# Kernel optimization log

Hardware: AMD Instinct MI355X
Metric: run time of the kernel (lower is better)

The kernel has to match this reference:

```python
import jax, jax.numpy as jnp
import numpy as np

D_MODEL = 1024
NUM_HEADS = 16
DEPTH = D_MODEL // NUM_HEADS


def setup_inputs() -> dict:
    key = jax.random.key(0)
    ks = jax.random.split(key, 10)
    B, LQ, LK = 4, 2048, 2048
    # xavier_uniform bound for square [d,d] weight
    bound = float(np.sqrt(6.0 / (D_MODEL + D_MODEL)))
    def w(k):
        return jax.random.uniform(k, (D_MODEL, D_MODEL), jnp.float32, -bound, bound)
    return {
        "query": jax.random.normal(ks[0], (B, LQ, D_MODEL), jnp.float32),
        "value": jax.random.normal(ks[1], (B, LK, D_MODEL), jnp.float32),
        "wq": w(ks[2]), "bq": jnp.zeros((D_MODEL,), jnp.float32),
        "wk": w(ks[3]), "bk": jnp.zeros((D_MODEL,), jnp.float32),
        "wv": w(ks[4]), "bv": jnp.zeros((D_MODEL,), jnp.float32),
        "wo": w(ks[5]), "bo": jnp.zeros((D_MODEL,), jnp.float32),
    }


def _split_heads(x, B):
    # [B, L, d_model] -> [B, H, L, depth]
    return x.reshape(B, -1, NUM_HEADS, DEPTH).transpose(0, 2, 1, 3)


def reference(query, value, wq, bq, wk, bk, wv, bv, wo, bo):
    B = query.shape[0]
    # torch nn.Linear: y = x @ W.T + b
    q = _split_heads(query @ wq.T + bq, B)          # [B,H,Lq,depth]
    k = _split_heads(value @ wk.T + bk, B)          # [B,H,Lk,depth]
    v = _split_heads(value @ wv.T + bv, B)          # [B,H,Lk,depth]
    scale = jnp.sqrt(jnp.asarray(DEPTH, dtype=q.dtype))
    scores = jnp.einsum("bhqd,bhkd->bhqk", q, k) / scale
    attn = jax.nn.softmax(scores, axis=-1)
    ctx = jnp.einsum("bhqk,bhkd->bhqd", attn, v)    # [B,H,Lq,depth]
    ctx = ctx.transpose(0, 2, 1, 3).reshape(B, -1, D_MODEL)
    return ctx @ wo.T + bo
```

## Files before the change

kernel.cpp:

```cpp
#include <hip/hip_runtime.h>
#include <hip/hip_bf16.h>

typedef unsigned short u16;
typedef unsigned int u32;
typedef __attribute__((ext_vector_type(8))) short bf16x8;
typedef __attribute__((ext_vector_type(4))) float f32x4;

#define MFMA16(a, b, c) __builtin_amdgcn_mfma_f32_16x16x32_bf16(a, b, c, 0, 0, 0)

#define QSCALE 0.18033688011112042f

__device__ inline u16 f2b(float f) {
    union { float f; unsigned int i; } v;
    v.f = f;
    unsigned int r = v.i + 0x7fffu + ((v.i >> 16) & 1u);
    return (u16)(r >> 16);
}
__device__ inline u32 fbits(float f) {
    union { float f; u32 i; } v; v.f = f; return v.i;
}
__device__ inline u32 pack2_trunc(float f0, float f1) {
    return __builtin_amdgcn_perm(fbits(f1), fbits(f0), 0x07060302u);
}

__device__ inline void glds16(const u16* g, u16* l) {
    __builtin_amdgcn_global_load_lds(
        (const __attribute__((address_space(1))) unsigned int*)g,
        (__attribute__((address_space(3))) unsigned int*)l, 16, 0, 0);
}

__global__ __launch_bounds__(256) void cvt_f32_bf16(
    const float* __restrict__ x, u16* __restrict__ y, int n)
{
    int i = (blockIdx.x * 256 + threadIdx.x) * 8;
    if (i >= n) return;
    float4 a = *(const float4*)(x + i);
    float4 b = *(const float4*)(x + i + 4);
    u16 o[8] = { f2b(a.x), f2b(a.y), f2b(a.z), f2b(a.w),
                 f2b(b.x), f2b(b.y), f2b(b.z), f2b(b.w) };
    *(uint4*)(y + i) = *(uint4*)o;
}

__global__ __launch_bounds__(256) void gemm_proj(
    const u16* __restrict__ qb, const u16* __restrict__ vb,
    const u16* __restrict__ wqb, const u16* __restrict__ wkb,
    const u16* __restrict__ wvb,
    const float* __restrict__ bq, const float* __restrict__ bk,
    const float* __restrict__ bv,
    u16* __restrict__ Qp, u16* __restrict__ Kp, u16* __restrict__ Vp,
    int M, int K)
{
    const int sel = blockIdx.y >> 3;
    const int n0 = (blockIdx.y & 7) * 128;
    const u16* A = sel ? vb : qb;
    const u16* W = sel == 0 ? wqb : (sel == 1 ? wkb : wvb);
    const float* bias = sel == 0 ? bq : (sel == 1 ? bk : bv);
    u16* C = sel == 0 ? Qp : (sel == 1 ? Kp : Vp);
    const float cscale = sel == 0 ? QSCALE : 1.0f;

    __shared__ __align__(16) u16 As[128 * 32];
    __shared__ __align__(16) u16 Bs[128 * 32];

    const int tid  = threadIdx.x;
    const int wave = tid >> 6, lane = tid & 63;
    const int quad = lane >> 4, l16 = lane & 15;
    const int m0 = blockIdx.x * 128;
    const int wm = (wave >> 1) * 64, wn = (wave & 1) * 64;
    const int r0 = lane >> 2;
    const int c0 = (lane & 3) * 8;

    f32x4 acc[4][4] = {};

    for (int k0 = 0; k0 < K; k0 += 32) {
        __syncthreads();
        {
            int ra = wave * 16 + r0;
            glds16(&A[(size_t)(m0 + ra) * K + k0 + c0],      &As[ra * 32 + c0]);
            glds16(&A[(size_t)(m0 + 64 + ra) * K + k0 + c0], &As[(64 + ra) * 32 + c0]);
            glds16(&W[(size_t)(n0 + ra) * K + k0 + c0],      &Bs[ra * 32 + c0]);
            glds16(&W[(size_t)(n0 + 64 + ra) * K + k0 + c0], &Bs[(64 + ra) * 32 + c0]);
        }
        __syncthreads();

        bf16x8 af[4], bfr[4];
#pragma unroll
        for (int mi = 0; mi < 4; ++mi)
            af[mi] = *(const bf16x8*)(&As[(wm + mi * 16 + l16) * 32 + quad * 8]);
#pragma unroll
        for (int ni = 0; ni < 4; ++ni)
            bfr[ni] = *(const bf16x8*)(&Bs[(wn + ni * 16 + l16) * 32 + quad * 8]);
#pragma unroll
        for (int mi = 0; mi < 4; ++mi)
#pragma unroll
            for (int ni = 0; ni < 4; ++ni)
                acc[mi][ni] = MFMA16(af[mi], bfr[ni], acc[mi][ni]);
    }

#pragma unroll
    for (int mi = 0; mi < 4; ++mi) {
#pragma unroll
        for (int ni = 0; ni < 4; ++ni) {
            int col = n0 + wn + ni * 16 + l16;
            float bv2 = bias[col];
#pragma unroll
            for (int r = 0; r < 4; ++r) {
                int row = m0 + wm + mi * 16 + quad * 4 + r;
                C[(size_t)row * 1024 + col] = f2b((acc[mi][ni][r] + bv2) * cscale);
            }
        }
    }
}

__global__ __launch_bounds__(256) void gemm_out(
    const u16* __restrict__ A, const u16* __restrict__ B,
    const float* __restrict__ bias, float* __restrict__ C,
    int M, int N, int K)
{
    __shared__ __align__(16) u16 As[128 * 32];
    __shared__ __align__(16) u16 Bs[128 * 32];

    const int tid  = threadIdx.x;
    const int wave = tid >> 6, lane = tid & 63;
    const int quad = lane >> 4, l16 = lane & 15;
    const int m0 = blockIdx.x * 128, n0 = blockIdx.y * 128;
    const int wm = (wave >> 1) * 64, wn = (wave & 1) * 64;
    const int r0 = lane >> 2;
    const int c0 = (lane & 3) * 8;

    f32x4 acc[4][4] = {};

    for (int k0 = 0; k0 < K; k0 += 32) {
        __syncthreads();
        {
            int ra = wave * 16 + r0;
            glds16(&A[(size_t)(m0 + ra) * K + k0 + c0],      &As[ra * 32 + c0]);
            glds16(&A[(size_t)(m0 + 64 + ra) * K + k0 + c0], &As[(64 + ra) * 32 + c0]);
            glds16(&B[(size_t)(n0 + ra) * K + k0 + c0],      &Bs[ra * 32 + c0]);
            glds16(&B[(size_t)(n0 + 64 + ra) * K + k0 + c0], &Bs[(64 + ra) * 32 + c0]);
        }
        __syncthreads();

        bf16x8 af[4], bfr[4];
#pragma unroll
        for (int mi = 0; mi < 4; ++mi)
            af[mi] = *(const bf16x8*)(&As[(wm + mi * 16 + l16) * 32 + quad * 8]);
#pragma unroll
        for (int ni = 0; ni < 4; ++ni)
            bfr[ni] = *(const bf16x8*)(&Bs[(wn + ni * 16 + l16) * 32 + quad * 8]);
#pragma unroll
        for (int mi = 0; mi < 4; ++mi)
#pragma unroll
            for (int ni = 0; ni < 4; ++ni)
                acc[mi][ni] = MFMA16(af[mi], bfr[ni], acc[mi][ni]);
    }

#pragma unroll
    for (int mi = 0; mi < 4; ++mi) {
#pragma unroll
        for (int ni = 0; ni < 4; ++ni) {
            int col = n0 + wn + ni * 16 + l16;
            float bv = bias[col];
#pragma unroll
            for (int r = 0; r < 4; ++r) {
                int row = m0 + wm + mi * 16 + quad * 4 + r;
                C[(size_t)row * N + col] = acc[mi][ni][r] + bv;
            }
        }
    }
}

__global__ __launch_bounds__(256) void transpose_v(
    const u16* __restrict__ Vp, u16* __restrict__ VT)
{
    __shared__ u16 T[64 * 66];
    const int tid = threadIdx.x;
    const int l0 = blockIdx.x * 64, d0 = blockIdx.y * 64, b = blockIdx.z;

#pragma unroll
    for (int i = 0; i < 2; ++i) {
        int ch = tid + i * 256;
        int lrow = ch >> 3, c8 = (ch & 7) * 8;
        uint4 vv = *(const uint4*)(&Vp[((size_t)b * 2048 + l0 + lrow) * 1024 + d0 + c8]);
        const u16* vp = (const u16*)&vv;
#pragma unroll
        for (int j = 0; j < 8; ++j) T[lrow * 66 + c8 + j] = vp[j];
    }
    __syncthreads();
#pragma unroll
    for (int i = 0; i < 2; ++i) {
        int ch = tid + i * 256;
        int drow = ch >> 3, l8 = (ch & 7) * 8;
        u16 o[8];
#pragma unroll
        for (int j = 0; j < 8; ++j) o[j] = T[(l8 + j) * 66 + drow];
        *(uint4*)(&VT[((size_t)b * 1024 + d0 + drow) * 2048 + l0 + l8]) = *(uint4*)o;
    }
}

__global__ __launch_bounds__(256) void attn(
    const u16* __restrict__ Q, const u16* __restrict__ K,
    const u16* __restrict__ VT, u16* __restrict__ O,
    int LQ, int LK)
{
    const int tid  = threadIdx.x;
    const int wave = tid >> 6, lane = tid & 63;
    const int quad = lane >> 4, l16 = lane & 15;
    const int q0 = blockIdx.x * 256;
    const int bh = blockIdx.y;
    const int b = bh >> 4, h = bh & 15;
    const size_t qbase = ((size_t)b * LQ + q0) * 1024 + h * 64;
    const size_t kbase = ((size_t)b * LK) * 1024 + h * 64;
    const size_t vtbase = ((size_t)b * 1024 + h * 64) * 2048;

    __shared__ __align__(16) u16 Ks[64 * 72];
    __shared__ __align__(16) u16 VTs[80 * 72];
    __shared__ __align__(16) u16 Ps[4][64 * 72];

    for (int i = tid; i < 16 * 72; i += 256) VTs[64 * 72 + i] = 0x3F80;

    bf16x8 qf[4][2];
#pragma unroll
    for (int mi = 0; mi < 4; ++mi)
#pragma unroll
        for (int ks = 0; ks < 2; ++ks)
            qf[mi][ks] = *(const bf16x8*)(
                &Q[qbase + (size_t)(wave * 64 + mi * 16 + l16) * 1024 + ks * 32 + quad * 8]);

    f32x4 oacc[4][5] = {};

    for (int kt = 0; kt < LK; kt += 64) {
        __syncthreads();
#pragma unroll
        for (int i = 0; i < 2; ++i) {
            int ch = tid + i * 256;
            int row = ch >> 3, c8 = (ch & 7) * 8;
            *(uint4*)(&Ks[row * 72 + c8]) =
                *(const uint4*)(&K[kbase + (size_t)(kt + row) * 1024 + c8]);
            *(uint4*)(&VTs[row * 72 + c8]) =
                *(const uint4*)(&VT[vtbase + (size_t)row * 2048 + kt + c8]);
        }
        __syncthreads();

        f32x4 st[4][4] = {};
#pragma unroll
        for (int ks = 0; ks < 2; ++ks) {
            bf16x8 kf[4];
#pragma unroll
            for (int ni = 0; ni < 4; ++ni)
                kf[ni] = *(const bf16x8*)(&Ks[(ni * 16 + l16) * 72 + ks * 32 + quad * 8]);
#pragma unroll
            for (int ni = 0; ni < 4; ++ni)
#pragma unroll
                for (int mi = 0; mi < 4; ++mi)
                    st[ni][mi] = MFMA16(kf[ni], qf[mi][ks], st[ni][mi]);
        }

#pragma unroll
        for (int mi = 0; mi < 4; ++mi)
#pragma unroll
            for (int ni = 0; ni < 4; ++ni) {
                float p0 = __builtin_amdgcn_exp2f(st[ni][mi][0]);
                float p1 = __builtin_amdgcn_exp2f(st[ni][mi][1]);
                float p2 = __builtin_amdgcn_exp2f(st[ni][mi][2]);
                float p3 = __builtin_amdgcn_exp2f(st[ni][mi][3]);
                uint2 w;
                w.x = pack2_trunc(p0, p1);
                w.y = pack2_trunc(p2, p3);
                *(uint2*)(&Ps[wave][(mi * 16 + l16) * 72 + ni * 16 + quad * 4]) = w;
            }

#pragma unroll
        for (int ks = 0; ks < 2; ++ks) {
            bf16x8 vf[5];
#pragma unroll
            for (int nd = 0; nd < 5; ++nd)
                vf[nd] = *(const bf16x8*)(&VTs[(nd * 16 + l16) * 72 + ks * 32 + quad * 8]);
#pragma unroll
            for (int mi = 0; mi < 4; ++mi) {
                bf16x8 pf = *(const bf16x8*)(&Ps[wave][(mi * 16 + l16) * 72 + ks * 32 + quad * 8]);
#pragma unroll
                for (int nd = 0; nd < 5; ++nd)
                    oacc[mi][nd] = MFMA16(pf, vf[nd], oacc[mi][nd]);
            }
        }
    }

#pragma unroll
    for (int mi = 0; mi < 4; ++mi)
#pragma unroll
        for (int r = 0; r < 4; ++r) {
            float inv = 1.0f / oacc[mi][4][r];
            int row = q0 + wave * 64 + mi * 16 + quad * 4 + r;
            size_t rb = ((size_t)b * LQ + row) * 1024 + h * 64;
#pragma unroll
            for (int nd = 0; nd < 4; ++nd)
                O[rb + nd * 16 + l16] = f2b(oacc[mi][nd][r] * inv);
        }
}

extern "C" void kernel_launch(void* const* d_in, const int* in_sizes, int n_in,
                              void* d_out, int out_size, void* d_ws, size_t ws_size,
                              hipStream_t stream) {
    const float* query = (const float*)d_in[0];
    const float* value = (const float*)d_in[1];
    const float* wq = (const float*)d_in[2];
    const float* bq = (const float*)d_in[3];
    const float* wk = (const float*)d_in[4];
    const float* bk = (const float*)d_in[5];
    const float* wv = (const float*)d_in[6];
    const float* bv = (const float*)d_in[7];
    const float* wo = (const float*)d_in[8];
    const float* bo = (const float*)d_in[9];

    const int B = 4, LQ = 2048, LK = 2048, D = 1024;
    const int M = B * LQ;
    const int mat = M * D;
    const int wsz = D * D;

    u16* ws  = (u16*)d_ws;
    u16* qb  = ws;
    u16* vb  = qb + mat;
    u16* wqb = vb + mat;
    u16* wkb = wqb + wsz;
    u16* wvb = wkb + wsz;
    u16* wob = wvb + wsz;
    u16* Qp  = wob + wsz;
    u16* Kp  = Qp + mat;
    u16* Vp  = Kp + mat;
    u16* VT  = Vp + mat;
    u16* Cp  = Vp;

    dim3 blk(256);

    cvt_f32_bf16<<<dim3(mat / 2048), blk, 0, stream>>>(query, qb, mat);
    cvt_f32_bf16<<<dim3(mat / 2048), blk, 0, stream>>>(value, vb, mat);
    cvt_f32_bf16<<<dim3(wsz / 2048), blk, 0, stream>>>(wq, wqb, wsz);
    cvt_f32_bf16<<<dim3(wsz / 2048), blk, 0, stream>>>(wk, wkb, wsz);
    cvt_f32_bf16<<<dim3(wsz / 2048), blk, 0, stream>>>(wv, wvb, wsz);
    cvt_f32_bf16<<<dim3(wsz / 2048), blk, 0, stream>>>(wo, wob, wsz);

    gemm_proj<<<dim3(M / 128, 24), blk, 0, stream>>>(
        qb, vb, wqb, wkb, wvb, bq, bk, bv, Qp, Kp, Vp, M, D);

    transpose_v<<<dim3(32, 16, 4), blk, 0, stream>>>(Vp, VT);

    attn<<<dim3(LQ / 256, B * 16), blk, 0, stream>>>(Qp, Kp, VT, Cp, LQ, LK);

    gemm_out<<<dim3(M / 128, D / 128), blk, 0, stream>>>(Cp, wob, bo, (float*)d_out, M, D, D);
}
```

Measured before the change: 349.5 us.

## Shrink attention tiles, remap blocks per XCD, fuse conversion launches

The attention kernel now gives each block 128 query rows (32 per wave) instead of 256. It uses smaller P buffers in shared memory and raises the occupancy hint to 4 blocks per SM. The row-sum column moves from shared memory into a register vector of ones, and a flat 1D grid maps blocks so each XCD works on neighbouring heads. s_setprio marks the MFMA sections, and six conversion launches are merged into two. Each block now reloads K/V for fewer queries, which doubles K/V traffic per query.

```diff
diff --git a/kernel.cpp b/kernel.cpp
--- a/kernel.cpp
+++ b/kernel.cpp
@@ -29,9 +29,30 @@
         (__attribute__((address_space(3))) unsigned int*)l, 16, 0, 0);
 }
 
-__global__ __launch_bounds__(256) void cvt_f32_bf16(
-    const float* __restrict__ x, u16* __restrict__ y, int n)
-{
+__global__ __launch_bounds__(256) void cvt2_f32_bf16(
+    const float* __restrict__ x0, const float* __restrict__ x1,
+    u16* __restrict__ y0, u16* __restrict__ y1, int n)
+{
+    const float* x = blockIdx.y ? x1 : x0;
+    u16* y = blockIdx.y ? y1 : y0;
+    int i = (blockIdx.x * 256 + threadIdx.x) * 8;
+    if (i >= n) return;
+    float4 a = *(const float4*)(x + i);
+    float4 b = *(const float4*)(x + i + 4);
+    u16 o[8] = { f2b(a.x), f2b(a.y), f2b(a.z), f2b(a.w),
+                 f2b(b.x), f2b(b.y), f2b(b.z), f2b(b.w) };
+    *(uint4*)(y + i) = *(uint4*)o;
+}
+
+__global__ __launch_bounds__(256) void cvt4_f32_bf16(
+    const float* __restrict__ x0, const float* __restrict__ x1,
+    const float* __restrict__ x2, const float* __restrict__ x3,
+    u16* __restrict__ y0, u16* __restrict__ y1,
+    u16* __restrict__ y2, u16* __restrict__ y3, int n)
+{
+    int s = blockIdx.y;
+    const float* x = s == 0 ? x0 : (s == 1 ? x1 : (s == 2 ? x2 : x3));
+    u16* y = s == 0 ? y0 : (s == 1 ? y1 : (s == 2 ? y2 : y3));
     int i = (blockIdx.x * 256 + threadIdx.x) * 8;
     if (i >= n) return;
     float4 a = *(const float4*)(x + i);
@@ -197,7 +218,7 @@
     }
 }
 
-__global__ __launch_bounds__(256) void attn(
+__global__ __launch_bounds__(256, 4) void attn(
     const u16* __restrict__ Q, const u16* __restrict__ K,
     const u16* __restrict__ VT, u16* __restrict__ O,
     int LQ, int LK)
@@ -205,28 +226,31 @@
     const int tid  = threadIdx.x;
     const int wave = tid >> 6, lane = tid & 63;
     const int quad = lane >> 4, l16 = lane & 15;
-    const int q0 = blockIdx.x * 256;
-    const int bh = blockIdx.y;
+    const int flat = blockIdx.x;
+    const int xcd = flat & 7, slot = flat >> 3;
+    const int bh = xcd * 8 + (slot >> 4);
+    const int q0 = (slot & 15) * 128;
     const int b = bh >> 4, h = bh & 15;
     const size_t qbase = ((size_t)b * LQ + q0) * 1024 + h * 64;
     const size_t kbase = ((size_t)b * LK) * 1024 + h * 64;
     const size_t vtbase = ((size_t)b * 1024 + h * 64) * 2048;
 
     __shared__ __align__(16) u16 Ks[64 * 72];
-    __shared__ __align__(16) u16 VTs[80 * 72];
-    __shared__ __align__(16) u16 Ps[4][64 * 72];
-
-    for (int i = tid; i < 16 * 72; i += 256) VTs[64 * 72 + i] = 0x3F80;
-
-    bf16x8 qf[4][2];
-#pragma unroll
-    for (int mi = 0; mi < 4; ++mi)
+    __shared__ __align__(16) u16 VTs[64 * 72];
+    __shared__ __align__(16) u16 Ps[4][32 * 40];
+
+    bf16x8 qf[2][2];
+#pragma unroll
+    for (int mi = 0; mi < 2; ++mi)
 #pragma unroll
         for (int ks = 0; ks < 2; ++ks)
             qf[mi][ks] = *(const bf16x8*)(
-                &Q[qbase + (size_t)(wave * 64 + mi * 16 + l16) * 1024 + ks * 32 + quad * 8]);
-
-    f32x4 oacc[4][5] = {};
+                &Q[qbase + (size_t)(wave * 32 + mi * 16 + l16) * 1024 + ks * 32 + quad * 8]);
+
+    const bf16x8 vones = { 0x3F80, 0x3F80, 0x3F80, 0x3F80,
+                           0x3F80, 0x3F80, 0x3F80, 0x3F80 };
+
+    f32x4 oacc[2][5] = {};
 
     for (int kt = 0; kt < LK; kt += 64) {
         __syncthreads();
@@ -241,56 +265,62 @@
         }
         __syncthreads();
 
-        f32x4 st[4][4] = {};
+        f32x4 st[4][2] = {};
 #pragma unroll
         for (int ks = 0; ks < 2; ++ks) {
             bf16x8 kf[4];
 #pragma unroll
             for (int ni = 0; ni < 4; ++ni)
                 kf[ni] = *(const bf16x8*)(&Ks[(ni * 16 + l16) * 72 + ks * 32 + quad * 8]);
+            __builtin_amdgcn_s_setprio(1);
 #pragma unroll
             for (int ni = 0; ni < 4; ++ni)
 #pragma unroll
-                for (int mi = 0; mi < 4; ++mi)
+                for (int mi = 0; mi < 2; ++mi)
                     st[ni][mi] = MFMA16(kf[ni], qf[mi][ks], st[ni][mi]);
-        }
-
-#pragma unroll
-        for (int mi = 0; mi < 4; ++mi)
-#pragma unroll
-            for (int ni = 0; ni < 4; ++ni) {
-                float p0 = __builtin_amdgcn_exp2f(st[ni][mi][0]);
-                float p1 = __builtin_amdgcn_exp2f(st[ni][mi][1]);
-                float p2 = __builtin_amdgcn_exp2f(st[ni][mi][2]);
-                float p3 = __builtin_amdgcn_exp2f(st[ni][mi][3]);
-                uint2 w;
-                w.x = pack2_trunc(p0, p1);
-                w.y = pack2_trunc(p2, p3);
-                *(uint2*)(&Ps[wave][(mi * 16 + l16) * 72 + ni * 16 + quad * 4]) = w;
+            __builtin_amdgcn_s_setprio(0);
+        }
+
+#pragma unroll
+        for (int ks = 0; ks < 2; ++ks) {
+#pragma unroll
+            for (int mi = 0; mi < 2; ++mi)
+#pragma unroll
+                for (int ni2 = 0; ni2 < 2; ++ni2) {
+                    const f32x4 s4 = st[ks * 2 + ni2][mi];
+                    float p0 = __builtin_amdgcn_exp2f(s4[0]);
+                    float p1 = __builtin_amdgcn_exp2f(s4[1]);
+                    float p2 = __builtin_amdgcn_exp2f(s4[2]);
+                    float p3 = __builtin_amdgcn_exp2f(s4[3]);
+                    uint2 w;
+                    w.x = pack2_trunc(p0, p1);
+                    w.y = pack2_trunc(p2, p3);
+                    *(uint2*)(&Ps[wave][(mi * 16 + l16) * 40 + ni2 * 16 + quad * 4]) = w;
+                }
+
+            bf16x8 vf[4];
+#pragma unroll
+            for (int nd = 0; nd < 4; ++nd)
+                vf[nd] = *(const bf16x8*)(&VTs[(nd * 16 + l16) * 72 + ks * 32 + quad * 8]);
+            __builtin_amdgcn_s_setprio(1);
+#pragma unroll
+            for (int mi = 0; mi < 2; ++mi) {
+                bf16x8 pf = *(const bf16x8*)(&Ps[wave][(mi * 16 + l16) * 40 + quad * 8]);
+#pragma unroll
+                for (int nd = 0; nd < 4; ++nd)
+                    oacc[mi][nd] = MFMA16(pf, vf[nd], oacc[mi][nd]);
+                oacc[mi][4] = MFMA16(pf, vones, oacc[mi][4]);
             }
-
-#pragma unroll
-        for (int ks = 0; ks < 2; ++ks) {
-            bf16x8 vf[5];
-#pragma unroll
-            for (int nd = 0; nd < 5; ++nd)
-                vf[nd] = *(const bf16x8*)(&VTs[(nd * 16 + l16) * 72 + ks * 32 + quad * 8]);
-#pragma unroll
-            for (int mi = 0; mi < 4; ++mi) {
-                bf16x8 pf = *(const bf16x8*)(&Ps[wave][(mi * 16 + l16) * 72 + ks * 32 + quad * 8]);
-#pragma unroll
-                for (int nd = 0; nd < 5; ++nd)
-                    oacc[mi][nd] = MFMA16(pf, vf[nd], oacc[mi][nd]);
-            }
-        }
-    }
-
-#pragma unroll
-    for (int mi = 0; mi < 4; ++mi)
+            __builtin_amdgcn_s_setprio(0);
+        }
+    }
+
+#pragma unroll
+    for (int mi = 0; mi < 2; ++mi)
 #pragma unroll
         for (int r = 0; r < 4; ++r) {
             float inv = 1.0f / oacc[mi][4][r];
-            int row = q0 + wave * 64 + mi * 16 + quad * 4 + r;
+            int row = q0 + wave * 32 + mi * 16 + quad * 4 + r;
             size_t rb = ((size_t)b * LQ + row) * 1024 + h * 64;
 #pragma unroll
             for (int nd = 0; nd < 4; ++nd)
@@ -332,19 +362,16 @@
 
     dim3 blk(256);
 
-    cvt_f32_bf16<<<dim3(mat / 2048), blk, 0, stream>>>(query, qb, mat);
-    cvt_f32_bf16<<<dim3(mat / 2048), blk, 0, stream>>>(value, vb, mat);
-    cvt_f32_bf16<<<dim3(wsz / 2048), blk, 0, stream>>>(wq, wqb, wsz);
-    cvt_f32_bf16<<<dim3(wsz / 2048), blk, 0, stream>>>(wk, wkb, wsz);
-    cvt_f32_bf16<<<dim3(wsz / 2048), blk, 0, stream>>>(wv, wvb, wsz);
-    cvt_f32_bf16<<<dim3(wsz / 2048), blk, 0, stream>>>(wo, wob, wsz);
+    cvt2_f32_bf16<<<dim3(mat / 2048, 2), blk, 0, stream>>>(query, value, qb, vb, mat);
+    cvt4_f32_bf16<<<dim3(wsz / 2048, 4), blk, 0, stream>>>(
+        wq, wk, wv, wo, wqb, wkb, wvb, wob, wsz);
 
     gemm_proj<<<dim3(M / 128, 24), blk, 0, stream>>>(
         qb, vb, wqb, wkb, wvb, bq, bk, bv, Qp, Kp, Vp, M, D);
 
     transpose_v<<<dim3(32, 16, 4), blk, 0, stream>>>(Vp, VT);
 
-    attn<<<dim3(LQ / 256, B * 16), blk, 0, stream>>>(Qp, Kp, VT, Cp, LQ, LK);
+    attn<<<dim3(1024), blk, 0, stream>>>(Qp, Kp, VT, Cp, LQ, LK);
 
     gemm_out<<<dim3(M / 128, D / 128), blk, 0, stream>>>(Cp, wob, bo, (float*)d_out, M, D, D);
 }
```

Result: faster. 323.6 us (-7.4%).
